# Performance work log

Hardware: AMD Instinct MI355X
Metric: run time of the kernel (lower is better)

## Reference

```python
import jax, jax.numpy as jnp
import numpy as np

B, T, H = 2, 2048, 1024
NUM_HEADS = 16
HEAD_DIM = H // NUM_HEADS
MAX_REL = 4


def setup_inputs() -> dict:
    key = jax.random.key(0)
    ks = jax.random.split(key, 12)
    s = 1.0 / np.sqrt(H)
    inp = {
        "x": jax.random.normal(ks[0], (B, T, H), dtype=jnp.float32),
        "text_mask": jax.random.randint(ks[1], (B, T), 0, 2, dtype=jnp.int32),
        "Wq": jax.random.normal(ks[2], (H, H), dtype=jnp.float32) * s,
        "bq": jnp.zeros((H,), dtype=jnp.float32),
        "Wk": jax.random.normal(ks[3], (H, H), dtype=jnp.float32) * s,
        "bk": jnp.zeros((H,), dtype=jnp.float32),
        "Wv": jax.random.normal(ks[4], (H, H), dtype=jnp.float32) * s,
        "bv": jnp.zeros((H,), dtype=jnp.float32),
        "Wo": jax.random.normal(ks[5], (H, H), dtype=jnp.float32) * s,
        "bo": jnp.zeros((H,), dtype=jnp.float32),
        "rel_bias": jax.random.normal(ks[6], (2 * MAX_REL + 1, NUM_HEADS), dtype=jnp.float32),
    }
    return inp


def reference(x, text_mask, Wq, bq, Wk, bk, Wv, bv, Wo, bo, rel_bias):
    b, t, h = x.shape
    scale = HEAD_DIM ** (-0.5)

    def proj(W, bias):
        # [b,t,h] -> [b,heads,t,head_dim]
        return (x @ W.T + bias).reshape(b, t, NUM_HEADS, HEAD_DIM).transpose(0, 2, 1, 3)

    q = proj(Wq, bq)
    k = proj(Wk, bk)
    v = proj(Wv, bv)

    scores = jnp.einsum("bhqd,bhkd->bhqk", q, k) * scale  # [b,heads,t,t]

    pos = jnp.arange(t)
    rel = jnp.clip(pos[None, :] - pos[:, None], -MAX_REL, MAX_REL) + MAX_REL  # [t,t]
    bias = rel_bias[rel]  # [t,t,heads]
    scores = scores + bias.transpose(2, 0, 1)[None]  # broadcast over batch

    key_valid = text_mask.astype(bool)  # [b,t]
    scores = jnp.where(key_valid[:, None, None, :], scores, -10000.0)

    attn = jax.nn.softmax(scores, axis=-1)
    hidden = jnp.einsum("bhqk,bhkd->bhqd", attn, v)
    hidden = hidden.transpose(0, 2, 1, 3).reshape(b, t, h)
    out = hidden @ Wo.T + bo
    return out * text_mask.astype(out.dtype)[:, :, None]
```

## Files before the change

### kernel.cpp

```cpp
#include <hip/hip_runtime.h>
#include <hip/hip_bf16.h>

#define B_ 2
#define T_ 2048
#define H_ 1024
#define NH 16
#define HD 64

typedef __attribute__((ext_vector_type(8))) short bf16x8;
typedef __attribute__((ext_vector_type(4))) short bf16x4;
typedef __attribute__((ext_vector_type(4))) float f32x4;

#define ASYNC_COPY16(gptr, lptr)                                              \
    __builtin_amdgcn_global_load_lds(                                         \
        (const __attribute__((address_space(1))) void*)(gptr),                \
        (__attribute__((address_space(3))) void*)(lptr), 16, 0, 0)

#if __has_builtin(__builtin_amdgcn_exp2f)
#define EXP2(x) __builtin_amdgcn_exp2f(x)
#else
static __device__ inline float EXP2(float x) {
    float r;
    asm volatile("v_exp_f32 %0, %1" : "=v"(r) : "v"(x));
    return r;
}
#endif

static __device__ inline unsigned short f2bf(float f) {
    union { float f; unsigned u; } v; v.f = f;
    unsigned r = v.u + 0x7fff + ((v.u >> 16) & 1);
    return (unsigned short)(r >> 16);
}

static __device__ inline unsigned pkbf(float a, float b) {
    float2 t2; t2.x = a; t2.y = b;
    __hip_bfloat162 h = __float22bfloat162_rn(t2);
    union { __hip_bfloat162 h; unsigned u; } cv; cv.h = h;
    return cv.u;
}

static __device__ inline bf16x8 mk8(unsigned a, unsigned b, unsigned c,
                                    unsigned d) {
    union { bf16x8 v; unsigned u[4]; } cv;
    cv.u[0] = a; cv.u[1] = b; cv.u[2] = c; cv.u[3] = d;
    return cv.v;
}

static __device__ inline f32x4 zero4() {
    f32x4 z = {0.f, 0.f, 0.f, 0.f};
    return z;
}

#define LOG2E 1.44269504088896f

__global__ void cvt_kernel(const float* __restrict__ x,
                           const float* __restrict__ wq,
                           const float* __restrict__ wk,
                           const float* __restrict__ wv,
                           const float* __restrict__ wo,
                           const int* __restrict__ maskp,
                           unsigned short* __restrict__ dst,
                           unsigned* __restrict__ cidx,
                           unsigned short* __restrict__ vidx,
                           unsigned short* __restrict__ maskc,
                           unsigned* __restrict__ meta,
                           float* __restrict__ outz) {
    if (blockIdx.x > 8192) {
        long long idx =
            ((long long)(blockIdx.x - 8193) * 256 + threadIdx.x) * 4;
        if (idx < 4194304LL) {
            float4 z = {0.f, 0.f, 0.f, 0.f};
            *(float4*)(outz + idx) = z;
        }
        return;
    }
    if (blockIdx.x == 8192) {
        __shared__ unsigned ps[256];
        int t = threadIdx.x;
        int base = t * 16;
        int bb = base >> 11;
        unsigned mv = 0, cnt = 0;
#pragma unroll
        for (int i = 0; i < 16; i++) {
            if (maskp[base + i]) { mv |= (1u << i); cnt++; }
        }
        ps[t] = cnt;
        __syncthreads();
        for (int off = 1; off < 128; off <<= 1) {
            unsigned add = ((t & 127) >= off) ? ps[t - off] : 0;
            __syncthreads();
            ps[t] += add;
            __syncthreads();
        }
        unsigned cnt0 = ps[127], cnt1 = ps[255];
        unsigned ex = ps[t] - cnt;
        unsigned local = ex;
        unsigned g = (bb ? cnt0 : 0) + ex;
        for (int i = 0; i < 16; i++) {
            if (mv & (1u << i)) {
                cidx[g] = (unsigned)(base + i);
                vidx[bb * 2048 + local] =
                    (unsigned short)(base + i - bb * 2048);
                maskc[bb * 2048 + local] = 0x3F80;
                g++; local++;
            }
        }
        if (t == 0) { meta[0] = cnt0; meta[1] = cnt1; meta[2] = cnt0 + cnt1; }
        __syncthreads();
        unsigned C = cnt0 + cnt1;
        for (unsigned i = C + t; i < 4224; i += 256) cidx[i] = 0;
        for (unsigned i = cnt0 + t; i < 2048; i += 256) {
            vidx[i] = 0; maskc[i] = 0;
        }
        for (unsigned i = cnt1 + t; i < 2048; i += 256) {
            vidx[2048 + i] = 0; maskc[2048 + i] = 0;
        }
        return;
    }
    long long i0 = ((long long)blockIdx.x * blockDim.x + threadIdx.x) * 4;
    const float* src; long long off;
    if (i0 < 4194304LL)      { src = x;  off = i0; }
    else if (i0 < 5242880LL) { src = wq; off = i0 - 4194304LL; }
    else if (i0 < 6291456LL) { src = wk; off = i0 - 5242880LL; }
    else if (i0 < 7340032LL) { src = wv; off = i0 - 6291456LL; }
    else                     { src = wo; off = i0 - 7340032LL; }
    float4 f = *(const float4*)(src + off);
    ushort4 o;
    o.x = f2bf(f.x); o.y = f2bf(f.y); o.z = f2bf(f.z); o.w = f2bf(f.w);
    *(ushort4*)(dst + i0) = o;
}

__global__ __launch_bounds__(256) void qkv_gemm(
    const unsigned short* __restrict__ A,
    const unsigned short* __restrict__ Bm,
    const float* __restrict__ bq, const float* __restrict__ bk,
    const float* __restrict__ bv,
    const unsigned* __restrict__ cidx, const unsigned* __restrict__ meta,
    unsigned short* __restrict__ qout, unsigned short* __restrict__ kout,
    unsigned short* __restrict__ vout) {
    const int K = 1024;
    int C  = (int)meta[2];
    int c0 = (int)meta[0];
    int m0 = blockIdx.y * 64, n0 = blockIdx.x * 128;
    if (m0 >= C) return;
    __shared__ __align__(16) unsigned short As[2][64 * 32];
    __shared__ __align__(16) unsigned short Bs[2][128 * 32];
    int t = threadIdx.x;
    int w = t >> 6, lane = t & 63;
    int wm = (w >> 1) * 32, wn = (w & 1) * 64;
    int c = lane & 15, qd = lane >> 4;

    f32x4 acc[2][4];
#pragma unroll
    for (int i = 0; i < 2; i++)
#pragma unroll
        for (int j = 0; j < 4; j++) acc[i][j] = zero4();

    int srow = t >> 2, sseg = (t & 3) * 8;
    int r1 = (int)cidx[m0 + srow];
    const unsigned short* ag1 = A + (long long)r1 * K + sseg;
    const unsigned short* bg1 = Bm + (long long)(n0 + srow) * K + sseg;
    const unsigned short* bg2 = bg1 + 64LL * K;

    for (int kk = 0; kk < K; kk += 64) {
        __syncthreads();
        ASYNC_COPY16(ag1 + kk,      &As[0][t * 8]);
        ASYNC_COPY16(ag1 + kk + 32, &As[1][t * 8]);
        ASYNC_COPY16(bg1 + kk,      &Bs[0][t * 8]);
        ASYNC_COPY16(bg1 + kk + 32, &Bs[1][t * 8]);
        ASYNC_COPY16(bg2 + kk,      &Bs[0][2048 + t * 8]);
        ASYNC_COPY16(bg2 + kk + 32, &Bs[1][2048 + t * 8]);
        __syncthreads();
#pragma unroll
        for (int p = 0; p < 2; p++) {
            bf16x8 af[2], bf[4];
#pragma unroll
            for (int i = 0; i < 2; i++)
                af[i] = *(const bf16x8*)(&As[p][(wm + i * 16 + c) * 32 +
                                                qd * 8]);
#pragma unroll
            for (int j = 0; j < 4; j++)
                bf[j] = *(const bf16x8*)(&Bs[p][(wn + j * 16 + c) * 32 +
                                                qd * 8]);
#pragma unroll
            for (int i = 0; i < 2; i++)
#pragma unroll
                for (int j = 0; j < 4; j++)
                    acc[i][j] = __builtin_amdgcn_mfma_f32_16x16x32_bf16(
                        af[i], bf[j], acc[i][j], 0, 0, 0);
        }
    }

    int gr[2][4];
#pragma unroll
    for (int i = 0; i < 2; i++)
#pragma unroll
        for (int r = 0; r < 4; r++) {
            int m = m0 + wm + i * 16 + qd * 4 + r;
            gr[i][r] = (m < C) ? (int)cidx[m] : -1;
        }

    const float QSCALE = 0.125f * LOG2E;
#pragma unroll
    for (int i = 0; i < 2; i++) {
        int m_base = m0 + wm + i * 16 + qd * 4;
#pragma unroll
        for (int j = 0; j < 4; j++) {
            int n = n0 + wn + j * 16 + c;
            int sel = n >> 10, within = n & 1023;
            int head = within >> 6, d = within & 63;
            if (sel == 0) {
                float ba = bq[within];
#pragma unroll
                for (int r = 0; r < 4; r++) {
                    if (gr[i][r] >= 0) {
                        int bb = gr[i][r] >> 11;
                        int loc = (m_base + r) - (bb ? c0 : 0);
                        qout[(((long long)(bb * NH + head)) * T_ + loc) * HD +
                             d] = f2bf((acc[i][j][r] + ba) * QSCALE);
                    }
                }
            } else if (sel == 1) {
                float ba = bk[within];
#pragma unroll
                for (int r = 0; r < 4; r++) {
                    if (gr[i][r] >= 0) {
                        int bb = gr[i][r] >> 11;
                        int loc = (m_base + r) - (bb ? c0 : 0);
                        kout[(((long long)(bb * NH + head)) * T_ + loc) * HD +
                             d] = f2bf(acc[i][j][r] + ba);
                    }
                }
            } else {
                float ba = bv[within];
                int g0 = gr[i][0], g3 = gr[i][3];
                int bb0 = g0 >> 11;
                int loc0 = m_base - (bb0 ? c0 : 0);
                if (g3 >= 0 && bb0 == (g3 >> 11) && ((loc0 & 3) == 0)) {
                    uint2 ov;
                    ov.x = pkbf(acc[i][j][0] + ba, acc[i][j][1] + ba);
                    ov.y = pkbf(acc[i][j][2] + ba, acc[i][j][3] + ba);
                    *(uint2*)(vout +
                              (((long long)(bb0 * NH + head)) * HD + d) * T_ +
                              loc0) = ov;
                } else {
#pragma unroll
                    for (int r = 0; r < 4; r++) {
                        if (gr[i][r] >= 0) {
                            int bb = gr[i][r] >> 11;
                            int loc = (m_base + r) - (bb ? c0 : 0);
                            vout[(((long long)(bb * NH + head)) * HD + d) *
                                     T_ +
                                 loc] = f2bf(acc[i][j][r] + ba);
                        }
                    }
                }
            }
        }
    }
}

__global__ __launch_bounds__(256) void out_gemm(
    const unsigned short* __restrict__ A,
    const unsigned short* __restrict__ Bm,
    const float* __restrict__ bo,
    const unsigned* __restrict__ cidx, const unsigned* __restrict__ meta,
    float* __restrict__ out) {
    const int K = 1024;
    int C = (int)meta[2];
    int m0 = blockIdx.y * 64, n0 = blockIdx.x * 64;
    if (m0 >= C) return;
    __shared__ __align__(16) unsigned short As[2][64 * 32];
    __shared__ __align__(16) unsigned short Bs[2][64 * 32];
    int t = threadIdx.x;
    int w = t >> 6, lane = t & 63;
    int wm = (w >> 1) * 32, wn = (w & 1) * 32;
    int c = lane & 15, qd = lane >> 4;

    f32x4 acc[2][2];
#pragma unroll
    for (int i = 0; i < 2; i++)
#pragma unroll
        for (int j = 0; j < 2; j++) acc[i][j] = zero4();

    int srow = t >> 2, sseg = (t & 3) * 8;
    int r1 = (int)cidx[m0 + srow];
    const unsigned short* ag1 = A + (long long)r1 * K + sseg;
    const unsigned short* bg1 = Bm + (long long)(n0 + srow) * K + sseg;

    for (int kk = 0; kk < K; kk += 64) {
        __syncthreads();
        ASYNC_COPY16(ag1 + kk,      &As[0][t * 8]);
        ASYNC_COPY16(ag1 + kk + 32, &As[1][t * 8]);
        ASYNC_COPY16(bg1 + kk,      &Bs[0][t * 8]);
        ASYNC_COPY16(bg1 + kk + 32, &Bs[1][t * 8]);
        __syncthreads();
#pragma unroll
        for (int p = 0; p < 2; p++) {
            bf16x8 af[2], bf[2];
#pragma unroll
            for (int i = 0; i < 2; i++)
                af[i] = *(const bf16x8*)(&As[p][(wm + i * 16 + c) * 32 +
                                                qd * 8]);
#pragma unroll
            for (int j = 0; j < 2; j++)
                bf[j] = *(const bf16x8*)(&Bs[p][(wn + j * 16 + c) * 32 +
                                                qd * 8]);
#pragma unroll
            for (int i = 0; i < 2; i++)
#pragma unroll
                for (int j = 0; j < 2; j++)
                    acc[i][j] = __builtin_amdgcn_mfma_f32_16x16x32_bf16(
                        af[i], bf[j], acc[i][j], 0, 0, 0);
        }
    }

#pragma unroll
    for (int i = 0; i < 2; i++) {
#pragma unroll
        for (int r = 0; r < 4; r++) {
            int m = m0 + wm + i * 16 + qd * 4 + r;
            if (m < C) {
                long long g = (long long)cidx[m];
#pragma unroll
                for (int j = 0; j < 2; j++) {
                    int n = n0 + wn + j * 16 + c;
                    out[g * 1024 + n] = acc[i][j][r] + bo[n];
                }
            }
        }
    }
}

__global__ __launch_bounds__(256, 2) void attn_kernel(
    const unsigned short* __restrict__ qg,
    const unsigned short* __restrict__ kg,
    const unsigned short* __restrict__ vTg,
    const float* __restrict__ rel_bias,
    const unsigned short* __restrict__ maskc,
    const unsigned short* __restrict__ vidxg,
    const unsigned* __restrict__ meta,
    unsigned short* __restrict__ hid) {
    int hb = blockIdx.x, qt = blockIdx.y;
    int h = hb & 15, b = hb >> 4;
    int cnt = (int)meta[b];
    if (qt * 64 >= cnt) return;
    int nkt = (cnt + 63) >> 6;
    int t = threadIdx.x, w = t >> 6, lane = t & 63;
    int c = lane & 15, qd = lane >> 4;

    __shared__ __align__(16) unsigned short lk[2][64 * 72];
    __shared__ __align__(16) unsigned short lvT[2][64 * 72];
    __shared__ __align__(16) unsigned short lmk[2][64];
    __shared__ __align__(16) unsigned short lki[2][64];
    __shared__ float lrbf[16];

    if (t < 9) lrbf[t] = rel_bias[t * 16 + h] * LOG2E;
    float rb0 = rel_bias[0 * 16 + h] * LOG2E;
    float rb8 = rel_bias[8 * 16 + h] * LOG2E;

    const unsigned short* qp =
        qg + (((long long)(b * NH + h)) * T_ + qt * 64) * HD;
    const unsigned short* kp = kg + ((long long)(b * NH + h)) * T_ * HD;
    const unsigned short* vp = vTg + ((long long)(b * NH + h)) * HD * T_;

    bf16x8 qf[2];
#pragma unroll
    for (int ks = 0; ks < 2; ks++)
        qf[ks] = *(const bf16x8*)(qp + (w * 16 + c) * HD + ks * 32 + qd * 8);

    const int imin = qt * 64 + w * 16;
    int imin_t = (int)vidxg[b * 2048 + min(imin, cnt - 1)];
    int imax_t = (int)vidxg[b * 2048 + min(imin + 15, cnt - 1)];
    int itrue = (int)vidxg[b * 2048 + min(imin + c, cnt - 1)];

    f32x4 o[4];
    f32x4 lacc;
#pragma unroll
    for (int dt = 0; dt < 4; dt++) o[dt] = zero4();
    lacc = zero4();

    int srow = t >> 2, sseg = (t & 3) * 16;
    int rr = srow & 15, hf = (srow >> 4) & 1;
    int gk = (srow & 32) + (rr >> 2) * 8 + hf * 4 + (rr & 3);
    const unsigned short* kst = kp + gk * HD + sseg;
    const unsigned short* vst = vp + srow * T_ + sseg;
    const unsigned short* mst = maskc + b * 2048 + t;
    const unsigned short* ist = vidxg + b * 2048 + t * 8;

    uint4 rk0 = *(const uint4*)(kst);
    uint4 rk1 = *(const uint4*)(kst + 8);
    uint4 rv0 = *(const uint4*)(vst);
    uint4 rv1 = *(const uint4*)(vst + 8);
    unsigned short rm = (t < 64) ? *mst : 0;
    uint4 rki = {0, 0, 0, 0};
    if (t < 8) rki = *(const uint4*)(ist);

    for (int kt = 0; kt < nkt; kt++) {
        unsigned short* KB = lk[kt & 1];
        unsigned short* VB = lvT[kt & 1];
        unsigned short* MK = lmk[kt & 1];
        unsigned short* KI = lki[kt & 1];
        *(uint4*)(KB + srow * 72 + sseg)     = rk0;
        *(uint4*)(KB + srow * 72 + sseg + 8) = rk1;
        *(uint4*)(VB + srow * 72 + sseg)     = rv0;
        *(uint4*)(VB + srow * 72 + sseg + 8) = rv1;
        if (t < 64) MK[t] = rm;
        if (t < 8) *(uint4*)(KI + t * 8) = rki;
        {
            int ktn = (kt < nkt - 1) ? kt + 1 : nkt - 1;
            rk0 = *(const uint4*)(kst + ktn * 64 * HD);
            rk1 = *(const uint4*)(kst + ktn * 64 * HD + 8);
            rv0 = *(const uint4*)(vst + ktn * 64);
            rv1 = *(const uint4*)(vst + ktn * 64 + 8);
            if (t < 64) rm = mst[ktn * 64];
            if (t < 8) rki = *(const uint4*)(ist + ktn * 64);
        }
        __syncthreads();

        int j0 = kt * 64;
        int jlo_t = (int)KI[0];
        int jhi_t = (int)KI[min(63, cnt - 1 - j0)];
        bool far_lo = (jhi_t <= imin_t - 4);
        bool far_hi = (jlo_t >= imax_t + 4);
        float ub = far_lo ? rb0 : rb8;
        bool nearband = !(far_lo || far_hi);

#pragma unroll
        for (int jp = 0; jp < 2; jp++) {
            int jb = jp * 32;
            const unsigned short* kbase = KB + (jb + c) * 72 + qd * 8;
            bf16x8 kfA0 = *(const bf16x8*)(kbase);
            bf16x8 kfA1 = *(const bf16x8*)(kbase + 32);
            bf16x8 kfB0 = *(const bf16x8*)(kbase + 16 * 72);
            bf16x8 kfB1 = *(const bf16x8*)(kbase + 16 * 72 + 32);
            bf16x8 m8 = *(const bf16x8*)(MK + jb + qd * 8);
            ushort4 kivA = *(const ushort4*)(KI + jb + qd * 8);
            ushort4 kivB = *(const ushort4*)(KI + jb + qd * 8 + 4);
            bf16x8 vf[4];
#pragma unroll
            for (int dt = 0; dt < 4; dt++)
                vf[dt] = *(const bf16x8*)(VB + (dt * 16 + c) * 72 + jb +
                                          qd * 8);
            f32x4 accA = zero4(), accB = zero4();
            accA = __builtin_amdgcn_mfma_f32_16x16x32_bf16(kfA0, qf[0], accA,
                                                           0, 0, 0);
            accA = __builtin_amdgcn_mfma_f32_16x16x32_bf16(kfA1, qf[1], accA,
                                                           0, 0, 0);
            accB = __builtin_amdgcn_mfma_f32_16x16x32_bf16(kfB0, qf[0], accB,
                                                           0, 0, 0);
            accB = __builtin_amdgcn_mfma_f32_16x16x32_bf16(kfB1, qf[1], accB,
                                                           0, 0, 0);
            float pA0, pA1, pA2, pA3, pB0, pB1, pB2, pB3;
            if (nearband) {
                int it = itrue;
                int a0 = (int)kivA.x - it;
                a0 = a0 < -4 ? -4 : (a0 > 4 ? 4 : a0);
                int a1 = (int)kivA.y - it;
                a1 = a1 < -4 ? -4 : (a1 > 4 ? 4 : a1);
                int a2 = (int)kivA.z - it;
                a2 = a2 < -4 ? -4 : (a2 > 4 ? 4 : a2);
                int a3 = (int)kivA.w - it;
                a3 = a3 < -4 ? -4 : (a3 > 4 ? 4 : a3);
                int b0i = (int)kivB.x - it;
                b0i = b0i < -4 ? -4 : (b0i > 4 ? 4 : b0i);
                int b1i = (int)kivB.y - it;
                b1i = b1i < -4 ? -4 : (b1i > 4 ? 4 : b1i);
                int b2i = (int)kivB.z - it;
                b2i = b2i < -4 ? -4 : (b2i > 4 ? 4 : b2i);
                int b3i = (int)kivB.w - it;
                b3i = b3i < -4 ? -4 : (b3i > 4 ? 4 : b3i);
                pA0 = EXP2(accA[0] + lrbf[a0 + 4]);
                pA1 = EXP2(accA[1] + lrbf[a1 + 4]);
                pA2 = EXP2(accA[2] + lrbf[a2 + 4]);
                pA3 = EXP2(accA[3] + lrbf[a3 + 4]);
                pB0 = EXP2(accB[0] + lrbf[b0i + 4]);
                pB1 = EXP2(accB[1] + lrbf[b1i + 4]);
                pB2 = EXP2(accB[2] + lrbf[b2i + 4]);
                pB3 = EXP2(accB[3] + lrbf[b3i + 4]);
            } else {
                pA0 = EXP2(accA[0] + ub);
                pA1 = EXP2(accA[1] + ub);
                pA2 = EXP2(accA[2] + ub);
                pA3 = EXP2(accA[3] + ub);
                pB0 = EXP2(accB[0] + ub);
                pB1 = EXP2(accB[1] + ub);
                pB2 = EXP2(accB[2] + ub);
                pB3 = EXP2(accB[3] + ub);
            }
            bf16x8 pf = mk8(pkbf(pA0, pA1), pkbf(pA2, pA3),
                            pkbf(pB0, pB1), pkbf(pB2, pB3));
            lacc = __builtin_amdgcn_mfma_f32_16x16x32_bf16(m8, pf, lacc, 0,
                                                           0, 0);
#pragma unroll
            for (int dt = 0; dt < 4; dt++)
                o[dt] = __builtin_amdgcn_mfma_f32_16x16x32_bf16(
                    vf[dt], pf, o[dt], 0, 0, 0);
        }
    }

    {
        int rc = imin + c;
        if (rc < cnt) {
            float invl = 1.0f / lacc[0];
            long long row = (long long)b * T_ + itrue;
#pragma unroll
            for (int dt = 0; dt < 4; dt++) {
                uint2 ov;
                ov.x = pkbf(o[dt][0] * invl, o[dt][1] * invl);
                ov.y = pkbf(o[dt][2] * invl, o[dt][3] * invl);
                *(uint2*)(hid + row * H_ + h * HD + dt * 16 + qd * 4) = ov;
            }
        }
    }
}

extern "C" void kernel_launch(void* const* d_in, const int* in_sizes, int n_in,
                              void* d_out, int out_size, void* d_ws,
                              size_t ws_size, hipStream_t stream) {
    const float* x    = (const float*)d_in[0];
    const int* maskp  = (const int*)d_in[1];
    const float* Wq   = (const float*)d_in[2];
    const float* bq   = (const float*)d_in[3];
    const float* Wk   = (const float*)d_in[4];
    const float* bk   = (const float*)d_in[5];
    const float* Wv   = (const float*)d_in[6];
    const float* bv   = (const float*)d_in[7];
    const float* Wo   = (const float*)d_in[8];
    const float* bo   = (const float*)d_in[9];
    const float* rb   = (const float*)d_in[10];
    float* out        = (float*)d_out;

    unsigned short* ws = (unsigned short*)d_ws;
    unsigned short* xb    = ws;
    unsigned short* wqkv  = ws + 4194304LL;
    unsigned short* wo_b  = ws + 7340032LL;
    unsigned short* qb    = ws + 8388608LL;
    unsigned short* kb    = ws + 12582912LL;
    unsigned short* vTb   = ws + 16777216LL;
    unsigned short* hid   = ws + 20971520LL;
    unsigned* meta        = (unsigned*)(ws + 25165824LL);
    unsigned* cidx        = (unsigned*)(ws + 25165856LL);
    unsigned short* vidx  = ws + 25174304LL;
    unsigned short* maskc = ws + 25178400LL;

    cvt_kernel<<<12289, 256, 0, stream>>>(x, Wq, Wk, Wv, Wo, maskp, ws, cidx,
                                          vidx, maskc, meta, out);
    qkv_gemm<<<dim3(24, 64), 256, 0, stream>>>(xb, wqkv, bq, bk, bv, cidx,
                                               meta, qb, kb, vTb);
    attn_kernel<<<dim3(32, 32), 256, 0, stream>>>(qb, kb, vTb, rb, maskc,
                                                  vidx, meta, hid);
    out_gemm<<<dim3(16, 64), 256, 0, stream>>>(hid, wo_b, bo, cidx, meta,
                                               out);
}
```

Measured before the change: 168.4 us.

## Double-buffer LDS tiles in QKV and output GEMMs to overlap loads with MFMA

Both projection GEMMs now keep two LDS stages and issue the async global-to-LDS copies for the next K-slice before computing the current one. Partial vmcnt waits and raw s_barrier replace the two __syncthreads per iteration, so memory latency can hide behind the matrix work. This doubles LDS use per block, which may lower occupancy. The hand-written waitcnt and barrier sequence also carries a risk of ordering hazards.

```diff
diff --git a/kernel.cpp b/kernel.cpp
--- a/kernel.cpp
+++ b/kernel.cpp
@@ -143,8 +143,8 @@
     int c0 = (int)meta[0];
     int m0 = blockIdx.y * 64, n0 = blockIdx.x * 128;
     if (m0 >= C) return;
-    __shared__ __align__(16) unsigned short As[2][64 * 32];
-    __shared__ __align__(16) unsigned short Bs[2][128 * 32];
+    __shared__ __align__(16) unsigned short As[2][2][64 * 32];
+    __shared__ __align__(16) unsigned short Bs[2][2][128 * 32];
     int t = threadIdx.x;
     int w = t >> 6, lane = t & 63;
     int wm = (w >> 1) * 32, wn = (w & 1) * 64;
@@ -162,26 +162,37 @@
     const unsigned short* bg1 = Bm + (long long)(n0 + srow) * K + sseg;
     const unsigned short* bg2 = bg1 + 64LL * K;
 
-    for (int kk = 0; kk < K; kk += 64) {
-        __syncthreads();
-        ASYNC_COPY16(ag1 + kk,      &As[0][t * 8]);
-        ASYNC_COPY16(ag1 + kk + 32, &As[1][t * 8]);
-        ASYNC_COPY16(bg1 + kk,      &Bs[0][t * 8]);
-        ASYNC_COPY16(bg1 + kk + 32, &Bs[1][t * 8]);
-        ASYNC_COPY16(bg2 + kk,      &Bs[0][2048 + t * 8]);
-        ASYNC_COPY16(bg2 + kk + 32, &Bs[1][2048 + t * 8]);
-        __syncthreads();
+#define QKV_STAGE(buf, kk)                                                    \
+    do {                                                                      \
+        ASYNC_COPY16(ag1 + (kk),      &As[buf][0][t * 8]);                    \
+        ASYNC_COPY16(ag1 + (kk) + 32, &As[buf][1][t * 8]);                    \
+        ASYNC_COPY16(bg1 + (kk),      &Bs[buf][0][t * 8]);                    \
+        ASYNC_COPY16(bg1 + (kk) + 32, &Bs[buf][1][t * 8]);                    \
+        ASYNC_COPY16(bg2 + (kk),      &Bs[buf][0][2048 + t * 8]);             \
+        ASYNC_COPY16(bg2 + (kk) + 32, &Bs[buf][1][2048 + t * 8]);             \
+    } while (0)
+
+    QKV_STAGE(0, 0);
+    for (int step = 0; step < 16; step++) {
+        int cur = step & 1;
+        if (step < 15) {
+            QKV_STAGE(cur ^ 1, (step + 1) * 64);
+            asm volatile("s_waitcnt vmcnt(6)" ::: "memory");
+        } else {
+            asm volatile("s_waitcnt vmcnt(0)" ::: "memory");
+        }
+        asm volatile("s_barrier" ::: "memory");
 #pragma unroll
         for (int p = 0; p < 2; p++) {
             bf16x8 af[2], bf[4];
 #pragma unroll
             for (int i = 0; i < 2; i++)
-                af[i] = *(const bf16x8*)(&As[p][(wm + i * 16 + c) * 32 +
-                                                qd * 8]);
+                af[i] = *(const bf16x8*)(&As[cur][p][(wm + i * 16 + c) * 32 +
+                                                     qd * 8]);
 #pragma unroll
             for (int j = 0; j < 4; j++)
-                bf[j] = *(const bf16x8*)(&Bs[p][(wn + j * 16 + c) * 32 +
-                                                qd * 8]);
+                bf[j] = *(const bf16x8*)(&Bs[cur][p][(wn + j * 16 + c) * 32 +
+                                                     qd * 8]);
 #pragma unroll
             for (int i = 0; i < 2; i++)
 #pragma unroll
@@ -189,7 +200,9 @@
                     acc[i][j] = __builtin_amdgcn_mfma_f32_16x16x32_bf16(
                         af[i], bf[j], acc[i][j], 0, 0, 0);
         }
-    }
+        asm volatile("s_barrier" ::: "memory");
+    }
+#undef QKV_STAGE
 
     int gr[2][4];
 #pragma unroll
@@ -270,8 +283,8 @@
     int C = (int)meta[2];
     int m0 = blockIdx.y * 64, n0 = blockIdx.x * 64;
     if (m0 >= C) return;
-    __shared__ __align__(16) unsigned short As[2][64 * 32];
-    __shared__ __align__(16) unsigned short Bs[2][64 * 32];
+    __shared__ __align__(16) unsigned short As[2][2][64 * 32];
+    __shared__ __align__(16) unsigned short Bs[2][2][64 * 32];
     int t = threadIdx.x;
     int w = t >> 6, lane = t & 63;
     int wm = (w >> 1) * 32, wn = (w & 1) * 32;
@@ -288,24 +301,35 @@
     const unsigned short* ag1 = A + (long long)r1 * K + sseg;
     const unsigned short* bg1 = Bm + (long long)(n0 + srow) * K + sseg;
 
-    for (int kk = 0; kk < K; kk += 64) {
-        __syncthreads();
-        ASYNC_COPY16(ag1 + kk,      &As[0][t * 8]);
-        ASYNC_COPY16(ag1 + kk + 32, &As[1][t * 8]);
-        ASYNC_COPY16(bg1 + kk,      &Bs[0][t * 8]);
-        ASYNC_COPY16(bg1 + kk + 32, &Bs[1][t * 8]);
-        __syncthreads();
+#define OUT_STAGE(buf, kk)                                                    \
+    do {                                                                      \
+        ASYNC_COPY16(ag1 + (kk),      &As[buf][0][t * 8]);                    \
+        ASYNC_COPY16(ag1 + (kk) + 32, &As[buf][1][t * 8]);                    \
+        ASYNC_COPY16(bg1 + (kk),      &Bs[buf][0][t * 8]);                    \
+        ASYNC_COPY16(bg1 + (kk) + 32, &Bs[buf][1][t * 8]);                    \
+    } while (0)
+
+    OUT_STAGE(0, 0);
+    for (int step = 0; step < 16; step++) {
+        int cur = step & 1;
+        if (step < 15) {
+            OUT_STAGE(cur ^ 1, (step + 1) * 64);
+            asm volatile("s_waitcnt vmcnt(4)" ::: "memory");
+        } else {
+            asm volatile("s_waitcnt vmcnt(0)" ::: "memory");
+        }
+        asm volatile("s_barrier" ::: "memory");
 #pragma unroll
         for (int p = 0; p < 2; p++) {
             bf16x8 af[2], bf[2];
 #pragma unroll
             for (int i = 0; i < 2; i++)
-                af[i] = *(const bf16x8*)(&As[p][(wm + i * 16 + c) * 32 +
-                                                qd * 8]);
+                af[i] = *(const bf16x8*)(&As[cur][p][(wm + i * 16 + c) * 32 +
+                                                     qd * 8]);
 #pragma unroll
             for (int j = 0; j < 2; j++)
-                bf[j] = *(const bf16x8*)(&Bs[p][(wn + j * 16 + c) * 32 +
-                                                qd * 8]);
+                bf[j] = *(const bf16x8*)(&Bs[cur][p][(wn + j * 16 + c) * 32 +
+                                                     qd * 8]);
 #pragma unroll
             for (int i = 0; i < 2; i++)
 #pragma unroll
@@ -313,7 +337,9 @@
                     acc[i][j] = __builtin_amdgcn_mfma_f32_16x16x32_bf16(
                         af[i], bf[j], acc[i][j], 0, 0, 0);
         }
-    }
+        asm volatile("s_barrier" ::: "memory");
+    }
+#undef OUT_STAGE
 
 #pragma unroll
     for (int i = 0; i < 2; i++) {
```

New measurement: 174.0 us. +3.3%, slower.
